# Kernel optimization log

Measured on AMD Instinct MI355X. Metric: run time of the kernel, lower is better.

The kernel has to match this reference:

```python
import jax, jax.numpy as jnp
import numpy as np

BN_EPS = 1e-5


def _bn(x, gamma, beta):
    # BatchNorm2d in training mode: batch statistics over (B, T, V) per channel.
    mean = jnp.mean(x, axis=(0, 2, 3), keepdims=True)
    var = jnp.var(x, axis=(0, 2, 3), keepdims=True)
    inv = jax.lax.rsqrt(var + BN_EPS)
    g = gamma[None, :, None, None]
    b = beta[None, :, None, None]
    return (x - mean) * inv * g + b


def setup_inputs() -> dict:
    key = jax.random.key(0)
    ks = jax.random.split(key, 8)
    B, Cin, Cout, T, V = 32, 64, 128, 300, 25
    x = jax.random.normal(ks[0], (B, Cin, T, V), dtype=jnp.float32)
    A_hat = jax.random.uniform(ks[1], (V, V), dtype=jnp.float32) / V  # row-normalized-ish adjacency
    # spatial 1x1 conv weight/bias
    w_sp = jax.random.normal(ks[2], (Cout, Cin), dtype=jnp.float32) * (1.0 / np.sqrt(Cin))
    b_sp = jnp.zeros((Cout,), dtype=jnp.float32)
    g_sp = jnp.ones((Cout,), dtype=jnp.float32)
    be_sp = jnp.zeros((Cout,), dtype=jnp.float32)
    # temporal conv (9,1) weight/bias, same channels
    w_t = jax.random.normal(ks[3], (Cout, Cout, 9, 1), dtype=jnp.float32) * (1.0 / np.sqrt(Cout * 9))
    b_t = jnp.zeros((Cout,), dtype=jnp.float32)
    g_t = jnp.ones((Cout,), dtype=jnp.float32)
    be_t = jnp.zeros((Cout,), dtype=jnp.float32)
    # residual 1x1 conv + BN (in_channels != out_channels)
    w_r = jax.random.normal(ks[4], (Cout, Cin), dtype=jnp.float32) * (1.0 / np.sqrt(Cin))
    b_r = jnp.zeros((Cout,), dtype=jnp.float32)
    g_r = jnp.ones((Cout,), dtype=jnp.float32)
    be_r = jnp.zeros((Cout,), dtype=jnp.float32)
    return {
        "x": x, "A_hat": A_hat,
        "w_sp": w_sp, "b_sp": b_sp, "g_sp": g_sp, "be_sp": be_sp,
        "w_t": w_t, "b_t": b_t, "g_t": g_t, "be_t": be_t,
        "w_r": w_r, "b_r": b_r, "g_r": g_r, "be_r": be_r,
    }


def reference(x, A_hat, w_sp, b_sp, g_sp, be_sp, w_t, b_t, g_t, be_t, w_r, b_r, g_r, be_r):
    # residual branch: 1x1 conv + BN
    res = jnp.einsum('oc,bctv->botv', w_r, x) + b_r[None, :, None, None]
    res = _bn(res, g_r, be_r)
    # spatial graph conv: A_hat @ x over node dim, then 1x1 conv
    h = jnp.einsum('vw,bctw->bctv', A_hat, x)
    h = jnp.einsum('oc,bctv->botv', w_sp, h) + b_sp[None, :, None, None]
    h = jax.nn.relu(_bn(h, g_sp, be_sp))
    # temporal conv (9,1) with padding (4,0), then BN
    h = jax.lax.conv_general_dilated(
        h, w_t, window_strides=(1, 1), padding=((4, 4), (0, 0)),
        dimension_numbers=('NCHW', 'OIHW', 'NCHW'))
    h = h + b_t[None, :, None, None]
    h = _bn(h, g_t, be_t)
    return jax.nn.relu(h + res)
```

## Files before the change

kernel.cpp:

```cpp
#include <hip/hip_runtime.h>

constexpr int B    = 32;
constexpr int CIN  = 64;
constexpr int COUT = 128;
constexpr int T    = 300;
constexpr int V    = 25;
constexpr int TV   = T * V;
constexpr long long NPC   = (long long)B * TV;
constexpr long long TOTAL = (long long)B * COUT * TV;

typedef short          bf16x8 __attribute__((ext_vector_type(8)));
typedef float          f32x4  __attribute__((ext_vector_type(4)));
typedef unsigned short us8    __attribute__((ext_vector_type(8)));
typedef unsigned short us4    __attribute__((ext_vector_type(4)));

static __device__ __forceinline__ unsigned short f2bf(float f) {
  union { float f; unsigned u; } x; x.f = f;
  unsigned r = x.u + 0x7FFFu + ((x.u >> 16) & 1u);
  return (unsigned short)(r >> 16);
}
static __device__ __forceinline__ float bf2f(unsigned short u) {
  union { unsigned u; float f; } x; x.u = ((unsigned)u) << 16;
  return x.f;
}

static __device__ __forceinline__ int xoff(int pos, int c) {
  return pos * 64 + ((((c >> 3)) ^ (pos & 7)) << 3) + (c & 7);
}
static __device__ __forceinline__ int soff(int c, int pw) {
  return c * 128 + ((((pw >> 3)) ^ (c & 7)) << 3) + (pw & 7);
}

__global__ __launch_bounds__(256) void kPrep(
    const float* __restrict__ w_t, const float* __restrict__ w_r,
    const float* __restrict__ w_sp, const float* __restrict__ A_hat,
    unsigned short* __restrict__ wb2, unsigned short* __restrict__ wrs2,
    unsigned short* __restrict__ bdt)
{
  int i = blockIdx.x * 256 + threadIdx.x;
  if (i < 147456) {
    int c = i & 127, ok = i >> 7;
    int k = ok % 9, o = ok / 9;
    int idx = ((k * 16 + (c >> 3)) * 128 + o) * 8 + (c & 7);
    wb2[idx] = f2bf(w_t[(o * COUT + c) * 9 + k]);
  } else if (i < 147456 + 16384) {
    int j = i - 147456;
    int c = j & 63, row = j >> 6;
    float v = (row < COUT) ? w_r[row * CIN + c] : w_sp[(row - COUT) * CIN + c];
    wrs2[((c >> 3) * 256 + row) * 8 + (c & 7)] = f2bf(v);
  } else {
    int j = i - 147456 - 16384;
    int pv = j >> 7, pw = j & 127;
    float v = 0.f;
    if (pv < 100 && pw < 100 && (pv / 25) == (pw / 25))
      v = A_hat[(pv % 25) * 25 + (pw % 25)];
    bdt[j] = f2bf(v);
  }
}

__global__ __launch_bounds__(256, 3) void kA4(
    const float* __restrict__ x, const unsigned short* __restrict__ bdt,
    const unsigned short* __restrict__ wrs2,
    unsigned short* __restrict__ resb, unsigned short* __restrict__ h,
    float2* __restrict__ part_rs)
{
  __shared__ unsigned short xs[64 * 128];
  __shared__ unsigned short xsp[112 * 64];
  __shared__ unsigned short axsp[112 * 64];

  const int tid  = threadIdx.x;
  const int lane = tid & 63;
  const int wave = tid >> 6;
  const int b    = blockIdx.y;
  const int p0   = blockIdx.x * 100;
  const int grp  = lane >> 4;
  const int l15  = lane & 15;

  for (int u = tid; u < 16 * 128; u += 256) {
    int pos = u & 127, c4 = u >> 7;
    int c0 = c4 * 4;
    float v0 = 0.f, v1 = 0.f, v2 = 0.f, v3 = 0.f;
    if (pos < 100) {
      const float* xp = &x[(b * CIN + c0) * TV + p0 + pos];
      v0 = xp[0]; v1 = xp[TV]; v2 = xp[2 * TV]; v3 = xp[3 * TV];
    }
    unsigned short b0 = f2bf(v0), b1 = f2bf(v1), b2 = f2bf(v2), b3 = f2bf(v3);
    xs[soff(c0,     pos)] = b0;
    xs[soff(c0 + 1, pos)] = b1;
    xs[soff(c0 + 2, pos)] = b2;
    xs[soff(c0 + 3, pos)] = b3;
    if (pos < 112) {
      us4 pk = {b0, b1, b2, b3};
      *(us4*)&xsp[xoff(pos, c0)] = pk;
    }
  }
  __syncthreads();

  bf16x8 xf[4];
#pragma unroll
  for (int ks = 0; ks < 4; ++ks)
    xf[ks] = *(const bf16x8*)&xs[soff(wave * 16 + l15, ks * 32 + grp * 8)];

  {
    f32x4 macc[7];
#pragma unroll
    for (int ni = 0; ni < 7; ++ni) macc[ni] = (f32x4)0.f;
    const int kst[7] = {0, 0, 0, 0, 1, 2, 2};
    const int kcn[7] = {1, 2, 2, 3, 3, 2, 2};
#pragma unroll
    for (int ni = 0; ni < 7; ++ni) {
      for (int kk = 0; kk < kcn[ni]; ++kk) {
        int ks = kst[ni] + kk;
        bf16x8 gf = *(const bf16x8*)&bdt[(ni * 16 + l15) * 128 + ks * 32 + grp * 8];
        macc[ni] = __builtin_amdgcn_mfma_f32_16x16x32_bf16(xf[ks], gf, macc[ni], 0, 0, 0);
      }
    }
#pragma unroll
    for (int ni = 0; ni < 7; ++ni) {
#pragma unroll
      for (int r = 0; r < 4; ++r)
        axsp[xoff(ni * 16 + l15, wave * 16 + grp * 4 + r)] = f2bf(macc[ni][r]);
    }
  }
  __syncthreads();

  const unsigned short* bsrc = (wave < 2) ? xsp : axsp;
  f32x4 acc[4][7];
#pragma unroll
  for (int m = 0; m < 4; ++m)
#pragma unroll
    for (int n = 0; n < 7; ++n) acc[m][n] = (f32x4)0.f;

#pragma unroll
  for (int ks = 0; ks < 2; ++ks) {
    bf16x8 af[4], bfr[7];
#pragma unroll
    for (int mi = 0; mi < 4; ++mi) {
      int row = wave * 64 + mi * 16 + l15;
      af[mi] = *(const bf16x8*)&wrs2[((ks * 4 + grp) * 256 + row) * 8];
    }
#pragma unroll
    for (int ni = 0; ni < 7; ++ni)
      bfr[ni] = *(const bf16x8*)&bsrc[xoff(ni * 16 + l15, ks * 32 + grp * 8)];
#pragma unroll
    for (int mi = 0; mi < 4; ++mi)
#pragma unroll
      for (int ni = 0; ni < 7; ++ni)
        acc[mi][ni] = __builtin_amdgcn_mfma_f32_16x16x32_bf16(
            af[mi], bfr[ni], acc[mi][ni], 0, 0, 0);
  }

  if (wave < 2) {
#pragma unroll
    for (int mi = 0; mi < 4; ++mi) {
#pragma unroll
      for (int ni = 0; ni < 7; ++ni) {
        int pos = ni * 16 + l15;
        if (pos < 100) {
#pragma unroll
          for (int r = 0; r < 4; ++r) {
            int c = wave * 64 + mi * 16 + grp * 4 + r;
            resb[((long long)(b * COUT + c)) * TV + p0 + pos] = f2bf(acc[mi][ni][r]);
          }
        }
      }
    }
  } else {
#pragma unroll
    for (int mi = 0; mi < 4; ++mi) {
      int o0 = (wave - 2) * 64 + mi * 16 + grp * 4;
#pragma unroll
      for (int ni = 0; ni < 7; ++ni) {
        int pos = ni * 16 + l15;
        if (pos < 100) {
          us4 pk;
#pragma unroll
          for (int r = 0; r < 4; ++r) pk[r] = f2bf(acc[mi][ni][r]);
          *(us4*)&h[((long long)(b * TV + p0 + pos)) * COUT + o0] = pk;
        }
      }
    }
  }

  {
    float2* pw = &part_rs[(((long long)(blockIdx.y * 75 + blockIdx.x)) * 4 + wave) * 64];
#pragma unroll
    for (int mi = 0; mi < 4; ++mi) {
#pragma unroll
      for (int r = 0; r < 4; ++r) {
        float s = 0.f, q = 0.f;
#pragma unroll
        for (int ni = 0; ni < 7; ++ni) {
          float v = (ni < 6 || l15 < 4) ? acc[mi][ni][r] : 0.f;
          s += v; q += v * v;
        }
#pragma unroll
        for (int m = 1; m < 16; m <<= 1) {
          s += __shfl_xor(s, m);
          q += __shfl_xor(q, m);
        }
        if (l15 == 0) pw[mi * 16 + grp * 4 + r] = make_float2(s, q);
      }
    }
  }
}

__global__ __launch_bounds__(256) void kC2v2(
    const float2* __restrict__ part_rs,
    const float* __restrict__ g_r,  const float* __restrict__ be_r,
    const float* __restrict__ g_sp, const float* __restrict__ be_sp,
    float* __restrict__ scales)
{
  __shared__ float rs[256], rq[256];
  const int row = blockIdx.x;
  const int wave = row >> 6, local = row & 63;
  const int tid = threadIdx.x;
  float s = 0.f, q = 0.f;
  for (int bid = tid; bid < 2400; bid += 256) {
    float2 v = part_rs[((long long)bid * 4 + wave) * 64 + local];
    s += v.x; q += v.y;
  }
  rs[tid] = s; rq[tid] = q;
  __syncthreads();
  for (int st = 128; st > 0; st >>= 1) {
    if (tid < st) { rs[tid] += rs[tid + st]; rq[tid] += rq[tid + st]; }
    __syncthreads();
  }
  if (tid == 0) {
    const float n = (float)NPC;
    float m = rs[0] / n, var = rq[0] / n - m * m;
    float iv = rsqrtf(var + 1e-5f);
    if (row < 128) {
      float sc = g_r[row] * iv;
      scales[row] = sc; scales[128 + row] = be_r[row] - m * sc;
    } else {
      int c = row - 128;
      float sc = g_sp[c] * iv;
      scales[256 + c] = sc; scales[384 + c] = be_sp[c] - m * sc;
    }
  }
}

constexpr int NP    = 256;
constexpr int HALO  = 100;
constexpr int STAGE = NP + 2 * HALO;

__global__ __launch_bounds__(512, 2) void kE7(
    const unsigned short* __restrict__ h, const unsigned short* __restrict__ wb2,
    const float* __restrict__ scales, unsigned short* __restrict__ cvb,
    float2* __restrict__ part_t)
{
  __shared__ unsigned short hs[STAGE * 64];
  const int tid  = threadIdx.x;
  const int lane = tid & 63;
  const int wave = tid >> 6;
  const int wm   = wave >> 2, wn = wave & 3;
  const int b    = blockIdx.y;
  const int p0   = blockIdx.x * NP;
  const int grp  = lane >> 4;
  const int l15  = lane & 15;
  const int slot = tid & 7;

  f32x4 acc[4][4];
#pragma unroll
  for (int m = 0; m < 4; ++m)
#pragma unroll
    for (int n = 0; n < 4; ++n) acc[m][n] = (f32x4)0.f;

  for (int cc = 0; cc < 2; ++cc) {
    if (cc) __syncthreads();
    const int c0 = cc * 64;
    float sc[8], sh[8];
#pragma unroll
    for (int e = 0; e < 8; ++e) {
      sc[e] = scales[256 + c0 + slot * 8 + e];
      sh[e] = scales[384 + c0 + slot * 8 + e];
    }
    for (int i = tid; i < STAGE * 8; i += 512) {
      int pos = i >> 3;
      int pg = p0 - HALO + pos;
      us8 o = (us8)(unsigned short)0;
      if (pg >= 0 && pg < TV) {
        us8 v = *(const us8*)&h[((long long)b * TV + pg) * COUT + c0 + slot * 8];
#pragma unroll
        for (int e = 0; e < 8; ++e)
          o[e] = f2bf(fmaxf(bf2f(v[e]) * sc[e] + sh[e], 0.f));
      }
      int si = (pos << 6) + ((slot ^ (pos & 7)) << 3);
      *(us8*)&hs[si] = o;
    }
    __syncthreads();

    __builtin_amdgcn_s_setprio(1);
    for (int k = 0; k < 9; ++k) {
      const int plb = HALO + wn * 64 + 25 * (k - 4) + l15;
#pragma unroll
      for (int ks = 0; ks < 2; ++ks) {
        bf16x8 af[4], bfr[4];
#pragma unroll
        for (int mi = 0; mi < 4; ++mi) {
          int o = wm * 64 + mi * 16 + l15;
          af[mi] = *(const bf16x8*)&wb2[((k * 16 + cc * 8 + ks * 4 + grp) * 128 + o) * 8];
        }
#pragma unroll
        for (int ni = 0; ni < 4; ++ni) {
          int pl = plb + ni * 16;
          int si = (pl << 6) + (((ks * 4 + grp) ^ (pl & 7)) << 3);
          bfr[ni] = *(const bf16x8*)&hs[si];
        }
#pragma unroll
        for (int mi = 0; mi < 4; ++mi)
#pragma unroll
          for (int ni = 0; ni < 4; ++ni)
            acc[mi][ni] = __builtin_amdgcn_mfma_f32_16x16x32_bf16(
                af[mi], bfr[ni], acc[mi][ni], 0, 0, 0);
      }
    }
    __builtin_amdgcn_s_setprio(0);
  }

#pragma unroll
  for (int mi = 0; mi < 4; ++mi) {
#pragma unroll
    for (int ni = 0; ni < 4; ++ni) {
      int pos = p0 + wn * 64 + ni * 16 + l15;
      if (pos < TV) {
#pragma unroll
        for (int r = 0; r < 4; ++r) {
          int o = wm * 64 + mi * 16 + grp * 4 + r;
          cvb[((long long)(b * COUT + o)) * TV + pos] = f2bf(acc[mi][ni][r]);
        }
      }
    }
  }

  {
    float2* pw = &part_t[(((long long)(blockIdx.y * 30 + blockIdx.x)) * 8 + wave) * 64];
#pragma unroll
    for (int mi = 0; mi < 4; ++mi) {
#pragma unroll
      for (int r = 0; r < 4; ++r) {
        float s = 0.f, q = 0.f;
#pragma unroll
        for (int ni = 0; ni < 4; ++ni) {
          int pos = p0 + wn * 64 + ni * 16 + l15;
          float v = (pos < TV) ? acc[mi][ni][r] : 0.f;
          s += v; q += v * v;
        }
#pragma unroll
        for (int m = 1; m < 16; m <<= 1) {
          s += __shfl_xor(s, m);
          q += __shfl_xor(q, m);
        }
        if (l15 == 0) pw[mi * 16 + grp * 4 + r] = make_float2(s, q);
      }
    }
  }
}

__global__ __launch_bounds__(256) void kG2(
    const float2* __restrict__ part_t,
    const float* __restrict__ g_t, const float* __restrict__ be_t,
    float* __restrict__ scales)
{
  __shared__ float rs[256], rq[256];
  const int c = blockIdx.x;
  const int wm = c >> 6, local = c & 63;
  const int tid = threadIdx.x;
  const int NB = 30 * 32;
  float s = 0.f, q = 0.f;
  for (int p = tid; p < NB * 4; p += 256) {
    int bid = p >> 2, wn = p & 3;
    float2 v = part_t[((long long)bid * 8 + (wm * 4 + wn)) * 64 + local];
    s += v.x; q += v.y;
  }
  rs[tid] = s; rq[tid] = q;
  __syncthreads();
  for (int st = 128; st > 0; st >>= 1) {
    if (tid < st) { rs[tid] += rs[tid + st]; rq[tid] += rq[tid + st]; }
    __syncthreads();
  }
  if (tid == 0) {
    const float n = (float)NPC;
    float m = rs[0] / n, var = rq[0] / n - m * m;
    float sc = g_t[c] * rsqrtf(var + 1e-5f);
    scales[512 + c] = sc;
    scales[640 + c] = be_t[c] - m * sc;
  }
}

__global__ __launch_bounds__(256) void kH(
    const unsigned short* __restrict__ cvb, const unsigned short* __restrict__ resb,
    const float* __restrict__ scales, float* __restrict__ out)
{
  const int plane = blockIdx.x;
  const int c = plane & 127;
  const float sct = scales[512 + c], sht = scales[640 + c];
  const float scr = scales[c],       shr = scales[128 + c];
  const us4* cp = (const us4*)&cvb[(long long)plane * TV];
  const us4* rp = (const us4*)&resb[(long long)plane * TV];
  float* op = &out[(long long)plane * TV];
  for (int u = threadIdx.x; u < 1875; u += 256) {
    us4 o4 = cp[u], r4 = rp[u];
    float4 y;
    y.x = fmaxf(bf2f(o4[0]) * sct + sht + bf2f(r4[0]) * scr + shr, 0.f);
    y.y = fmaxf(bf2f(o4[1]) * sct + sht + bf2f(r4[1]) * scr + shr, 0.f);
    y.z = fmaxf(bf2f(o4[2]) * sct + sht + bf2f(r4[2]) * scr + shr, 0.f);
    y.w = fmaxf(bf2f(o4[3]) * sct + sht + bf2f(r4[3]) * scr + shr, 0.f);
    *(float4*)&op[u * 4] = y;
  }
}

extern "C" void kernel_launch(void* const* d_in, const int* in_sizes, int n_in,
                              void* d_out, int out_size, void* d_ws, size_t ws_size,
                              hipStream_t stream) {
  const float* x     = (const float*)d_in[0];
  const float* A_hat = (const float*)d_in[1];
  const float* w_sp  = (const float*)d_in[2];
  const float* g_sp  = (const float*)d_in[4];
  const float* be_sp = (const float*)d_in[5];
  const float* w_t   = (const float*)d_in[6];
  const float* g_t   = (const float*)d_in[8];
  const float* be_t  = (const float*)d_in[9];
  const float* w_r   = (const float*)d_in[10];
  const float* g_r   = (const float*)d_in[12];
  const float* be_r  = (const float*)d_in[13];
  float* out = (float*)d_out;

  unsigned short* base_us = (unsigned short*)d_ws;
  unsigned short* resb = base_us;
  unsigned short* h    = base_us + (size_t)TOTAL;
  unsigned short* cvb  = base_us + (size_t)(2 * TOTAL);
  unsigned short* wb2  = base_us + (size_t)(3 * TOTAL);
  unsigned short* wrs2 = wb2 + 147456;
  unsigned short* bdt  = wrs2 + 16384;
  float2* part_rs = (float2*)(bdt + 14336);
  float2* part_t  = part_rs + 2400 * 4 * 64;
  float*  scales  = (float*)(part_t + 960 * 8 * 64);

  kPrep<<<696, 256, 0, stream>>>(w_t, w_r, w_sp, A_hat, wb2, wrs2, bdt);
  kA4<<<dim3(75, 32), 256, 0, stream>>>(x, bdt, wrs2, resb, h, part_rs);
  kC2v2<<<256, 256, 0, stream>>>(part_rs, g_r, be_r, g_sp, be_sp, scales);
  kE7<<<dim3(30, 32), 512, 0, stream>>>(h, wb2, scales, cvb, part_t);
  kG2<<<128, 256, 0, stream>>>(part_t, g_t, be_t, scales);
  kH<<<4096, 256, 0, stream>>>(cvb, resb, scales, out);
}
```

Before: 249.9 us.

## Switch intermediates to channel-last, shrink temporal tiles, reuse LDS, transpose in epilogue

The residual and conv outputs are now stored position-major with channels contiguous, so the epilogues write packed 4-channel vectors instead of scattered scalars. The final kernel reads 8-channel vectors and transposes back to NCHW fp32. The GCN kernel aliases one shared buffer to raise occupancy, and the BN partial-sum shuffle reduction becomes a transposed butterfly that needs one store per lane. The temporal-conv tile drops from 256 to 192 positions with higher occupancy bounds, which adds more blocks and more halo re-reads.

```diff
diff --git a/kernel.cpp b/kernel.cpp
--- a/kernel.cpp
+++ b/kernel.cpp
@@ -58,7 +58,7 @@
   }
 }
 
-__global__ __launch_bounds__(256, 3) void kA4(
+__global__ __launch_bounds__(256, 5) void kA5(
     const float* __restrict__ x, const unsigned short* __restrict__ bdt,
     const unsigned short* __restrict__ wrs2,
     unsigned short* __restrict__ resb, unsigned short* __restrict__ h,
@@ -66,7 +66,7 @@
 {
   __shared__ unsigned short xs[64 * 128];
   __shared__ unsigned short xsp[112 * 64];
-  __shared__ unsigned short axsp[112 * 64];
+  unsigned short* axsp = xs;
 
   const int tid  = threadIdx.x;
   const int lane = tid & 63;
@@ -100,6 +100,7 @@
 #pragma unroll
   for (int ks = 0; ks < 4; ++ks)
     xf[ks] = *(const bf16x8*)&xs[soff(wave * 16 + l15, ks * 32 + grp * 8)];
+  __syncthreads();
 
   {
     f32x4 macc[7];
@@ -150,25 +151,11 @@
             af[mi], bfr[ni], acc[mi][ni], 0, 0, 0);
   }
 
-  if (wave < 2) {
+  {
+    unsigned short* dst = (wave < 2) ? resb : h;
 #pragma unroll
     for (int mi = 0; mi < 4; ++mi) {
-#pragma unroll
-      for (int ni = 0; ni < 7; ++ni) {
-        int pos = ni * 16 + l15;
-        if (pos < 100) {
-#pragma unroll
-          for (int r = 0; r < 4; ++r) {
-            int c = wave * 64 + mi * 16 + grp * 4 + r;
-            resb[((long long)(b * COUT + c)) * TV + p0 + pos] = f2bf(acc[mi][ni][r]);
-          }
-        }
-      }
-    }
-  } else {
-#pragma unroll
-    for (int mi = 0; mi < 4; ++mi) {
-      int o0 = (wave - 2) * 64 + mi * 16 + grp * 4;
+      const int c0 = (wave & 1) * 64 + mi * 16 + grp * 4;
 #pragma unroll
       for (int ni = 0; ni < 7; ++ni) {
         int pos = ni * 16 + l15;
@@ -176,16 +163,16 @@
           us4 pk;
 #pragma unroll
           for (int r = 0; r < 4; ++r) pk[r] = f2bf(acc[mi][ni][r]);
-          *(us4*)&h[((long long)(b * TV + p0 + pos)) * COUT + o0] = pk;
+          *(us4*)&dst[((long long)(b * TV + p0 + pos)) * COUT + c0] = pk;
         }
       }
     }
   }
 
   {
-    float2* pw = &part_rs[(((long long)(blockIdx.y * 75 + blockIdx.x)) * 4 + wave) * 64];
-#pragma unroll
-    for (int mi = 0; mi < 4; ++mi) {
+    float sv[16], qv[16];
+#pragma unroll
+    for (int mi = 0; mi < 4; ++mi)
 #pragma unroll
       for (int r = 0; r < 4; ++r) {
         float s = 0.f, q = 0.f;
@@ -194,14 +181,25 @@
           float v = (ni < 6 || l15 < 4) ? acc[mi][ni][r] : 0.f;
           s += v; q += v * v;
         }
-#pragma unroll
-        for (int m = 1; m < 16; m <<= 1) {
-          s += __shfl_xor(s, m);
-          q += __shfl_xor(q, m);
-        }
-        if (l15 == 0) pw[mi * 16 + grp * 4 + r] = make_float2(s, q);
-      }
-    }
+        sv[mi * 4 + r] = s; qv[mi * 4 + r] = q;
+      }
+#pragma unroll
+    for (int bm = 1; bm < 16; bm <<= 1) {
+      const bool up = (l15 & bm) != 0;
+#pragma unroll
+      for (int i = 0; i < 16; i += 2 * bm) {
+        const int j = i + bm;
+        float ssend = up ? sv[i] : sv[j];
+        float qsend = up ? qv[i] : qv[j];
+        float sgot = __shfl_xor(ssend, bm);
+        float qgot = __shfl_xor(qsend, bm);
+        sv[i] = (up ? sv[j] : sv[i]) + sgot;
+        qv[i] = (up ? qv[j] : qv[i]) + qgot;
+      }
+    }
+    int slot = ((l15 >> 2) * 16) + grp * 4 + (l15 & 3);
+    float2* pw = &part_rs[(((long long)(blockIdx.y * 75 + blockIdx.x)) * 4 + wave) * 64];
+    pw[slot] = make_float2(sv[0], qv[0]);
   }
 }
 
@@ -241,11 +239,11 @@
   }
 }
 
-constexpr int NP    = 256;
+constexpr int NP    = 192;
 constexpr int HALO  = 100;
 constexpr int STAGE = NP + 2 * HALO;
 
-__global__ __launch_bounds__(512, 2) void kE7(
+__global__ __launch_bounds__(512, 6) void kE8(
     const unsigned short* __restrict__ h, const unsigned short* __restrict__ wb2,
     const float* __restrict__ scales, unsigned short* __restrict__ cvb,
     float2* __restrict__ part_t)
@@ -261,11 +259,11 @@
   const int l15  = lane & 15;
   const int slot = tid & 7;
 
-  f32x4 acc[4][4];
+  f32x4 acc[4][3];
 #pragma unroll
   for (int m = 0; m < 4; ++m)
 #pragma unroll
-    for (int n = 0; n < 4; ++n) acc[m][n] = (f32x4)0.f;
+    for (int n = 0; n < 3; ++n) acc[m][n] = (f32x4)0.f;
 
   for (int cc = 0; cc < 2; ++cc) {
     if (cc) __syncthreads();
@@ -293,17 +291,17 @@
 
     __builtin_amdgcn_s_setprio(1);
     for (int k = 0; k < 9; ++k) {
-      const int plb = HALO + wn * 64 + 25 * (k - 4) + l15;
+      const int plb = HALO + wn * 48 + 25 * (k - 4) + l15;
 #pragma unroll
       for (int ks = 0; ks < 2; ++ks) {
-        bf16x8 af[4], bfr[4];
+        bf16x8 af[4], bfr[3];
 #pragma unroll
         for (int mi = 0; mi < 4; ++mi) {
           int o = wm * 64 + mi * 16 + l15;
           af[mi] = *(const bf16x8*)&wb2[((k * 16 + cc * 8 + ks * 4 + grp) * 128 + o) * 8];
         }
 #pragma unroll
-        for (int ni = 0; ni < 4; ++ni) {
+        for (int ni = 0; ni < 3; ++ni) {
           int pl = plb + ni * 16;
           int si = (pl << 6) + (((ks * 4 + grp) ^ (pl & 7)) << 3);
           bfr[ni] = *(const bf16x8*)&hs[si];
@@ -311,7 +309,7 @@
 #pragma unroll
         for (int mi = 0; mi < 4; ++mi)
 #pragma unroll
-          for (int ni = 0; ni < 4; ++ni)
+          for (int ni = 0; ni < 3; ++ni)
             acc[mi][ni] = __builtin_amdgcn_mfma_f32_16x16x32_bf16(
                 af[mi], bfr[ni], acc[mi][ni], 0, 0, 0);
       }
@@ -321,40 +319,51 @@
 
 #pragma unroll
   for (int mi = 0; mi < 4; ++mi) {
-#pragma unroll
-    for (int ni = 0; ni < 4; ++ni) {
-      int pos = p0 + wn * 64 + ni * 16 + l15;
+    const int c0 = wm * 64 + mi * 16 + grp * 4;
+#pragma unroll
+    for (int ni = 0; ni < 3; ++ni) {
+      int pos = p0 + wn * 48 + ni * 16 + l15;
       if (pos < TV) {
-#pragma unroll
-        for (int r = 0; r < 4; ++r) {
-          int o = wm * 64 + mi * 16 + grp * 4 + r;
-          cvb[((long long)(b * COUT + o)) * TV + pos] = f2bf(acc[mi][ni][r]);
-        }
+        us4 pk;
+#pragma unroll
+        for (int r = 0; r < 4; ++r) pk[r] = f2bf(acc[mi][ni][r]);
+        *(us4*)&cvb[((long long)(b * TV + pos)) * COUT + c0] = pk;
       }
     }
   }
 
   {
-    float2* pw = &part_t[(((long long)(blockIdx.y * 30 + blockIdx.x)) * 8 + wave) * 64];
-#pragma unroll
-    for (int mi = 0; mi < 4; ++mi) {
+    float sv[16], qv[16];
+#pragma unroll
+    for (int mi = 0; mi < 4; ++mi)
 #pragma unroll
       for (int r = 0; r < 4; ++r) {
         float s = 0.f, q = 0.f;
 #pragma unroll
-        for (int ni = 0; ni < 4; ++ni) {
-          int pos = p0 + wn * 64 + ni * 16 + l15;
+        for (int ni = 0; ni < 3; ++ni) {
+          int pos = p0 + wn * 48 + ni * 16 + l15;
           float v = (pos < TV) ? acc[mi][ni][r] : 0.f;
           s += v; q += v * v;
         }
-#pragma unroll
-        for (int m = 1; m < 16; m <<= 1) {
-          s += __shfl_xor(s, m);
-          q += __shfl_xor(q, m);
-        }
-        if (l15 == 0) pw[mi * 16 + grp * 4 + r] = make_float2(s, q);
-      }
-    }
+        sv[mi * 4 + r] = s; qv[mi * 4 + r] = q;
+      }
+#pragma unroll
+    for (int bm = 1; bm < 16; bm <<= 1) {
+      const bool up = (l15 & bm) != 0;
+#pragma unroll
+      for (int i = 0; i < 16; i += 2 * bm) {
+        const int j = i + bm;
+        float ssend = up ? sv[i] : sv[j];
+        float qsend = up ? qv[i] : qv[j];
+        float sgot = __shfl_xor(ssend, bm);
+        float qgot = __shfl_xor(qsend, bm);
+        sv[i] = (up ? sv[j] : sv[i]) + sgot;
+        qv[i] = (up ? qv[j] : qv[i]) + qgot;
+      }
+    }
+    int slt = ((l15 >> 2) * 16) + grp * 4 + (l15 & 3);
+    float2* pw = &part_t[(((long long)(blockIdx.y * 40 + blockIdx.x)) * 8 + wave) * 64];
+    pw[slt] = make_float2(sv[0], qv[0]);
   }
 }
 
@@ -367,7 +376,7 @@
   const int c = blockIdx.x;
   const int wm = c >> 6, local = c & 63;
   const int tid = threadIdx.x;
-  const int NB = 30 * 32;
+  const int NB = 40 * 32;
   float s = 0.f, q = 0.f;
   for (int p = tid; p < NB * 4; p += 256) {
     int bid = p >> 2, wn = p & 3;
@@ -389,25 +398,42 @@
   }
 }
 
-__global__ __launch_bounds__(256) void kH(
+__global__ __launch_bounds__(256) void kH2(
     const unsigned short* __restrict__ cvb, const unsigned short* __restrict__ resb,
     const float* __restrict__ scales, float* __restrict__ out)
 {
-  const int plane = blockIdx.x;
-  const int c = plane & 127;
-  const float sct = scales[512 + c], sht = scales[640 + c];
-  const float scr = scales[c],       shr = scales[128 + c];
-  const us4* cp = (const us4*)&cvb[(long long)plane * TV];
-  const us4* rp = (const us4*)&resb[(long long)plane * TV];
-  float* op = &out[(long long)plane * TV];
-  for (int u = threadIdx.x; u < 1875; u += 256) {
-    us4 o4 = cp[u], r4 = rp[u];
-    float4 y;
-    y.x = fmaxf(bf2f(o4[0]) * sct + sht + bf2f(r4[0]) * scr + shr, 0.f);
-    y.y = fmaxf(bf2f(o4[1]) * sct + sht + bf2f(r4[1]) * scr + shr, 0.f);
-    y.z = fmaxf(bf2f(o4[2]) * sct + sht + bf2f(r4[2]) * scr + shr, 0.f);
-    y.w = fmaxf(bf2f(o4[3]) * sct + sht + bf2f(r4[3]) * scr + shr, 0.f);
-    *(float4*)&op[u * 4] = y;
+  const int tid  = threadIdx.x;
+  const int lane = tid & 63;
+  const int unit = blockIdx.x * 4 + (tid >> 6);
+  const int pt   = unit % 30;
+  const int rest = unit / 30;
+  const int cslot = rest & 15;
+  const int b    = rest >> 4;
+  const int c0   = cslot * 8;
+  float sct[8], sht[8], scr[8], shr[8];
+#pragma unroll
+  for (int e = 0; e < 8; ++e) {
+    sct[e] = scales[512 + c0 + e]; sht[e] = scales[640 + c0 + e];
+    scr[e] = scales[c0 + e];       shr[e] = scales[128 + c0 + e];
+  }
+  const int pbase = pt * 256 + lane * 4;
+  if (pbase + 4 > TV) return;
+  float y[4][8];
+#pragma unroll
+  for (int j = 0; j < 4; ++j) {
+    long long row = ((long long)b * TV + (pbase + j)) * COUT + c0;
+    us8 cv = *(const us8*)&cvb[row];
+    us8 rv = *(const us8*)&resb[row];
+#pragma unroll
+    for (int e = 0; e < 8; ++e)
+      y[j][e] = fmaxf(bf2f(cv[e]) * sct[e] + sht[e] +
+                      bf2f(rv[e]) * scr[e] + shr[e], 0.f);
+  }
+  float* ob = &out[((long long)b * COUT + c0) * TV + pbase];
+#pragma unroll
+  for (int e = 0; e < 8; ++e) {
+    float4 y4 = make_float4(y[0][e], y[1][e], y[2][e], y[3][e]);
+    *(float4*)&ob[(long long)e * TV] = y4;
   }
 }
 
@@ -436,12 +462,12 @@
   unsigned short* bdt  = wrs2 + 16384;
   float2* part_rs = (float2*)(bdt + 14336);
   float2* part_t  = part_rs + 2400 * 4 * 64;
-  float*  scales  = (float*)(part_t + 960 * 8 * 64);
+  float*  scales  = (float*)(part_t + 1280 * 8 * 64);
 
   kPrep<<<696, 256, 0, stream>>>(w_t, w_r, w_sp, A_hat, wb2, wrs2, bdt);
-  kA4<<<dim3(75, 32), 256, 0, stream>>>(x, bdt, wrs2, resb, h, part_rs);
+  kA5<<<dim3(75, 32), 256, 0, stream>>>(x, bdt, wrs2, resb, h, part_rs);
   kC2v2<<<256, 256, 0, stream>>>(part_rs, g_r, be_r, g_sp, be_sp, scales);
-  kE7<<<dim3(30, 32), 512, 0, stream>>>(h, wb2, scales, cvb, part_t);
+  kE8<<<dim3(40, 32), 512, 0, stream>>>(h, wb2, scales, cvb, part_t);
   kG2<<<128, 256, 0, stream>>>(part_t, g_t, be_t, scales);
-  kH<<<4096, 256, 0, stream>>>(cvb, resb, scales, out);
-}
+  kH2<<<3840, 256, 0, stream>>>(cvb, resb, scales, out);
+}
```

Result: slower. 546.0 us (+118.5%).
